# Performance work log

Measured on AMD Instinct MI355X. Metric: run time of the kernel, lower is better.

## Reference

```python
import jax, jax.numpy as jnp
import numpy as np

B, T, S, E, H, L, V = 32, 64, 64, 512, 1024, 2, 32000


def setup_inputs() -> dict:
    key = jax.random.key(0)
    ks = jax.random.split(key, 20)
    std = 0.02
    inp = {
        "x": jax.random.randint(ks[0], (B, T), 0, V),
        "h0": jax.random.normal(ks[1], (L, B, H), jnp.float32) * std,
        "c0": jax.random.normal(ks[2], (L, B, H), jnp.float32) * std,
        "x_enc": jax.random.normal(ks[3], (B, S, H), jnp.float32),
        "emb": jax.random.normal(ks[4], (V, E), jnp.float32) * std,
        # layer 0: input = concat(emb, prev_out) -> E + H
        "Wih0": jax.random.normal(ks[5], (4 * H, E + H), jnp.float32) * std,
        "Whh0": jax.random.normal(ks[6], (4 * H, H), jnp.float32) * std,
        "bih0": jnp.zeros((4 * H,), jnp.float32),
        "bhh0": jnp.zeros((4 * H,), jnp.float32),
        # layer 1: input = h of layer 0 -> H
        "Wih1": jax.random.normal(ks[7], (4 * H, H), jnp.float32) * std,
        "Whh1": jax.random.normal(ks[8], (4 * H, H), jnp.float32) * std,
        "bih1": jnp.zeros((4 * H,), jnp.float32),
        "bhh1": jnp.zeros((4 * H,), jnp.float32),
        # attention linear H->H
        "Wa": jax.random.normal(ks[9], (H, H), jnp.float32) * std,
        "ba": jnp.zeros((H,), jnp.float32),
        # output linear 2H->H
        "Wl": jax.random.normal(ks[10], (H, 2 * H), jnp.float32) * std,
        "bl": jnp.zeros((H,), jnp.float32),
        # generator H->V
        "Wg": jax.random.normal(ks[11], (V, H), jnp.float32) * std,
        "bg": jnp.zeros((V,), jnp.float32),
    }
    return inp


def _decoder_fwd(x, h0, c0, x_enc, emb, Wih0, Whh0, bih0, bhh0,
                 Wih1, Whh1, bih1, bhh1, Wa, ba, Wl, bl, Wg, bg):
    layers = ((Wih0, Whh0, bih0, bhh0), (Wih1, Whh1, bih1, bhh1))
    xs = emb[x]  # [B, T, E]

    def lstm_cell(inp, h_prev, c_prev, Wih, Whh, bih, bhh):
        g = inp @ Wih.T + bih + h_prev @ Whh.T + bhh  # [B, 4H]
        i_, f_, g_, o_ = jnp.split(g, 4, axis=-1)     # torch order: i,f,g,o
        c_new = jax.nn.sigmoid(f_) * c_prev + jax.nn.sigmoid(i_) * jnp.tanh(g_)
        h_new = jax.nn.sigmoid(o_) * jnp.tanh(c_new)
        return h_new, c_new

    def step(carry, e_t):
        h, c, prev = carry  # h,c: [L,B,H]; prev: [B,H]
        inp = jnp.concatenate([e_t, prev], axis=-1)  # [B, E+H]
        hs, cs = [], []
        for l, (Wih, Whh, bih, bhh) in enumerate(layers):
            h_new, c_new = lstm_cell(inp, h[l], c[l], Wih, Whh, bih, bhh)
            hs.append(h_new); cs.append(c_new)
            inp = h_new
        z = inp  # top-layer hidden [B, H]
        # attention: score = linear(z) . x_enc^T
        s = jnp.einsum('bh,bsh->bs', z @ Wa.T + ba, x_enc)  # [B, S]
        w = jax.nn.softmax(s, axis=-1)
        ctx = jnp.einsum('bs,bsh->bh', w, x_enc)            # [B, H]
        out = jnp.tanh(jnp.concatenate([z, ctx], axis=-1) @ Wl.T + bl)  # [B, H]
        return (jnp.stack(hs), jnp.stack(cs), out), out

    prev0 = jnp.zeros((x.shape[0], Wl.shape[0]), xs.dtype)
    e_seq = jnp.swapaxes(xs[:, :-1, :], 0, 1)  # [T-1, B, E]
    _, outs = jax.lax.scan(step, (h0, c0, prev0), e_seq)
    outs = jnp.swapaxes(outs, 0, 1)  # [B, T-1, H]
    # dropout p=0.0 (eval) -> identity; generator: linear + log_softmax
    return jax.nn.log_softmax(outs @ Wg.T + bg, axis=-1)  # [B, T-1, V]


def reference(x, h0, c0, x_enc, emb, Wih0, Whh0, bih0, bhh0,
              Wih1, Whh1, bih1, bhh1, Wa, ba, Wl, bl, Wg, bg):
    return _decoder_fwd(x, h0, c0, x_enc, emb, Wih0, Whh0, bih0, bhh0,
                        Wih1, Whh1, bih1, bhh1, Wa, ba, Wl, bl, Wg, bg)
```

## Files before the change

### kernel.cpp

```cpp
#include <hip/hip_runtime.h>
#include <hip/hip_cooperative_groups.h>
#include <math.h>

namespace cg = cooperative_groups;

#define BB 32
#define HH 1024
#define EE 512
#define TT 63
#define SS 64
#define VV 32000

static const size_t OWT0 = 0;
static const size_t OWT1 = 10485760;
static const size_t OWLT = 18874368;
static const size_t OXC0 = 20971520;
static const size_t OXC1 = 26214400;
static const size_t OGP  = 30408704;
static const size_t OOP  = 34603008;
static const size_t OPE  = 35651584;
static const size_t OCB  = 37748736;

__device__ __forceinline__ void fma4(float4& a, float s, const float4 w) {
    a.x = fmaf(s, w.x, a.x);
    a.y = fmaf(s, w.y, a.y);
    a.z = fmaf(s, w.z, a.z);
    a.w = fmaf(s, w.w, a.w);
}

template<int WPITCH, int NRT>
__device__ __forceinline__ void pgemm(const float* __restrict__ W,
                                      const float* __restrict__ X, int xpitch,
                                      int kslice, float* __restrict__ P)
{
    const int tid = threadIdx.x, lane = tid & 63, wv = tid >> 6;
    const int nU = NRT * 32;
    for (int u = blockIdx.x; u < nU; u += gridDim.x) {
        const int rt = u >> 5, kg = u & 31;
        const int r0 = rt * 256 + lane * 4;
        const int b0 = wv * 8;
        const int kbase = kg * kslice;
        const float* wb = W + (size_t)kbase * WPITCH + r0;
        const float* xb = X + (size_t)b0 * xpitch + kbase;
        float4 acc[8];
        #pragma unroll
        for (int i = 0; i < 8; ++i) acc[i] = make_float4(0.f, 0.f, 0.f, 0.f);
        #pragma unroll 2
        for (int kk = 0; kk < kslice; kk += 4) {
            float4 w0 = *(const float4*)(wb + (size_t)(kk + 0) * WPITCH);
            float4 w1 = *(const float4*)(wb + (size_t)(kk + 1) * WPITCH);
            float4 w2 = *(const float4*)(wb + (size_t)(kk + 2) * WPITCH);
            float4 w3 = *(const float4*)(wb + (size_t)(kk + 3) * WPITCH);
            #pragma unroll
            for (int i = 0; i < 8; ++i) {
                float4 xv = *(const float4*)(xb + (size_t)i * xpitch + kk);
                fma4(acc[i], xv.x, w0);
                fma4(acc[i], xv.y, w1);
                fma4(acc[i], xv.z, w2);
                fma4(acc[i], xv.w, w3);
            }
        }
        float* pp = P + ((size_t)kg * BB + b0) * WPITCH + r0;
        #pragma unroll
        for (int i = 0; i < 8; ++i) *(float4*)(pp + (size_t)i * WPITCH) = acc[i];
    }
}

__device__ __forceinline__ void lstm_fin(const float* __restrict__ P,
    const float* __restrict__ bih, const float* __restrict__ bhh,
    float* __restrict__ cst,
    float* __restrict__ hA, int pA, int oA,
    float* __restrict__ hB, int pB, int oB,
    float* __restrict__ smem)
{
    const int tid = threadIdx.x, lane = tid & 63, g = tid >> 6;
    for (int u = blockIdx.x; u < 512; u += gridDim.x) {
        const int b = u >> 4, hc = u & 15;
        const int h = hc * 64 + lane;
        float s = 0.f;
        #pragma unroll
        for (int sl = 0; sl < 32; ++sl)
            s += P[((size_t)sl * BB + b) * 4096 + g * 1024 + h];
        s += bih[g * 1024 + h] + bhh[g * 1024 + h];
        smem[g * 64 + lane] = s;
        __syncthreads();
        if (tid < 64) {
            float gi = smem[lane], gf = smem[64 + lane];
            float gg = smem[128 + lane], go = smem[192 + lane];
            float si = 1.f / (1.f + expf(-gi));
            float sf = 1.f / (1.f + expf(-gf));
            float so = 1.f / (1.f + expf(-go));
            float cp = cst[(size_t)b * 1024 + h];
            float cn = sf * cp + si * tanhf(gg);
            float hn = so * tanhf(cn);
            cst[(size_t)b * 1024 + h] = cn;
            hA[(size_t)b * pA + oA + h] = hn;
            hB[(size_t)b * pB + oB + h] = hn;
        }
        __syncthreads();
    }
}

__device__ __forceinline__ void attn_phase(const float* __restrict__ xenc,
    const float* __restrict__ pe, const float* __restrict__ cb,
    float* __restrict__ zc, float* __restrict__ smem)
{
    const int tid = threadIdx.x;
    float* zl = smem;
    float* pp = smem + 1024;
    float* wt = smem + 1280;
    for (int u = blockIdx.x; u < 32; u += gridDim.x) {
        const int b = u;
        for (int i = tid; i < 1024; i += 256) zl[i] = zc[(size_t)b * 2048 + i];
        __syncthreads();
        {
            const int j = tid >> 2, part = tid & 3;
            const float* per = pe + ((size_t)b * 64 + j) * 1024 + part * 256;
            const float* zp = zl + part * 256;
            float p0 = 0.f, p1 = 0.f, p2 = 0.f, p3 = 0.f;
            for (int k = 0; k < 256; k += 4) {
                p0 = fmaf(zp[k], per[k], p0);
                p1 = fmaf(zp[k + 1], per[k + 1], p1);
                p2 = fmaf(zp[k + 2], per[k + 2], p2);
                p3 = fmaf(zp[k + 3], per[k + 3], p3);
            }
            pp[tid] = (p0 + p1) + (p2 + p3);
        }
        __syncthreads();
        if (tid < 64) {
            float sc = pp[tid * 4] + pp[tid * 4 + 1] + pp[tid * 4 + 2] + pp[tid * 4 + 3]
                     + cb[b * 64 + tid];
            float m = sc;
            #pragma unroll
            for (int off = 32; off; off >>= 1) m = fmaxf(m, __shfl_xor(m, off));
            float e = expf(sc - m);
            float ss = e;
            #pragma unroll
            for (int off = 32; off; off >>= 1) ss += __shfl_xor(ss, off);
            wt[tid] = e / ss;
        }
        __syncthreads();
        for (int k = tid; k < 1024; k += 256) {
            float a = 0.f;
            const float* xe = xenc + (size_t)b * (SS * HH) + k;
            #pragma unroll 8
            for (int j = 0; j < SS; ++j) a = fmaf(wt[j], xe[(size_t)j * HH], a);
            zc[(size_t)b * 2048 + 1024 + k] = a;
        }
        __syncthreads();
    }
}

__device__ __forceinline__ void out_fin(const float* __restrict__ P,
    const float* __restrict__ bl, float* __restrict__ outs_t,
    float* __restrict__ xc0n, float* __restrict__ smem)
{
    const int tid = threadIdx.x, lane = tid & 63, wv = tid >> 6;
    for (int u = blockIdx.x; u < 512; u += gridDim.x) {
        const int b = u >> 4, nc = u & 15;
        const int n = nc * 64 + lane;
        float s = 0.f;
        #pragma unroll
        for (int q = 0; q < 8; ++q)
            s += P[((size_t)(wv * 8 + q) * BB + b) * 1024 + n];
        smem[wv * 64 + lane] = s;
        __syncthreads();
        if (tid < 64) {
            float tot = smem[lane] + smem[64 + lane] + smem[128 + lane]
                      + smem[192 + lane] + bl[n];
            float r = tanhf(tot);
            outs_t[(size_t)b * 1024 + n] = r;
            xc0n[(size_t)b * 2560 + 512 + n] = r;
        }
        __syncthreads();
    }
}

__global__ __launch_bounds__(256, 2)
void decoder_loop(const float* __restrict__ xenc,
                  const float* __restrict__ bih0, const float* __restrict__ bhh0,
                  const float* __restrict__ bih1, const float* __restrict__ bhh1,
                  const float* __restrict__ bl,
                  float* __restrict__ scratch,
                  float* __restrict__ c_state, float* __restrict__ zc,
                  float* __restrict__ outs)
{
    __shared__ float smem[1344];
    cg::grid_group grid = cg::this_grid();
    const float* WT0 = scratch + OWT0;
    const float* WT1 = scratch + OWT1;
    const float* WlT = scratch + OWLT;
    float* xcat0 = scratch + OXC0;
    float* xcat1 = scratch + OXC1;
    float* gatesP = scratch + OGP;
    float* outP = scratch + OOP;
    const float* pe = scratch + OPE;
    const float* cb = scratch + OCB;

    for (int t = 0; t < TT; ++t) {
        float* xc0t = xcat0 + (size_t)t * BB * 2560;
        float* xc0n = xcat0 + (size_t)(t + 1) * BB * 2560;
        float* xc1t = xcat1 + (size_t)t * BB * 2048;
        float* xc1n = xcat1 + (size_t)(t + 1) * BB * 2048;

        pgemm<4096, 16>(WT0, xc0t, 2560, 80, gatesP);
        grid.sync();
        lstm_fin(gatesP, bih0, bhh0, c_state,
                 xc1t, 2048, 0, xc0n, 2560, 1536, smem);
        grid.sync();
        pgemm<4096, 16>(WT1, xc1t, 2048, 64, gatesP);
        grid.sync();
        lstm_fin(gatesP, bih1, bhh1, c_state + 32768,
                 zc, 2048, 0, xc1n, 2048, 1024, smem);
        grid.sync();
        attn_phase(xenc, pe, cb, zc, smem);
        grid.sync();
        pgemm<1024, 4>(WlT, zc, 2048, 64, outP);
        grid.sync();
        out_fin(outP, bl, outs + (size_t)t * BB * HH, xc0n, smem);
        grid.sync();
    }
}

__global__ __launch_bounds__(256, 2)
void k_gate_gemm(const float* __restrict__ W, const float* __restrict__ X,
                 int xpitch, int kslice, float* __restrict__ P)
{ pgemm<4096, 16>(W, X, xpitch, kslice, P); }

__global__ __launch_bounds__(256, 2)
void k_out_gemm(const float* __restrict__ W, const float* __restrict__ X,
                float* __restrict__ P)
{ pgemm<1024, 4>(W, X, 2048, 64, P); }

__global__ __launch_bounds__(256)
void k_lstm_fin(const float* __restrict__ P, const float* __restrict__ bih,
                const float* __restrict__ bhh, float* __restrict__ cst,
                float* __restrict__ hA, int pA, int oA,
                float* __restrict__ hB, int pB, int oB)
{ __shared__ float smem[256]; lstm_fin(P, bih, bhh, cst, hA, pA, oA, hB, pB, oB, smem); }

__global__ __launch_bounds__(256)
void k_attn(const float* __restrict__ xenc, const float* __restrict__ pe,
            const float* __restrict__ cb, float* __restrict__ zc)
{ __shared__ float smem[1344]; attn_phase(xenc, pe, cb, zc, smem); }

__global__ __launch_bounds__(256)
void k_out_fin(const float* __restrict__ P, const float* __restrict__ bl,
               float* __restrict__ outs_t, float* __restrict__ xc0n)
{ __shared__ float smem[256]; out_fin(P, bl, outs_t, xc0n, smem); }

__global__ __launch_bounds__(256)
void init_kernel2(const float* __restrict__ h0, const float* __restrict__ c0,
                  float* __restrict__ c_state, float* __restrict__ xcat0,
                  float* __restrict__ xcat1)
{
    int i = blockIdx.x * 256 + threadIdx.x;
    c_state[i] = c0[i];
    int b = (i >> 10) & 31, h = i & 1023, l = i >> 15;
    if (l == 0) {
        xcat0[(size_t)b * 2560 + 1536 + h] = h0[i];
        xcat0[(size_t)b * 2560 + 512 + h] = 0.f;
    } else {
        xcat1[(size_t)b * 2048 + 1024 + h] = h0[i];
    }
}

__global__ __launch_bounds__(128)
void embed_kernel2(const int* __restrict__ x, const float* __restrict__ emb,
                   float* __restrict__ xcat0)
{
    int t = blockIdx.x >> 5, b = blockIdx.x & 31;
    int tok = x[b * 64 + t];
    const float4* src = (const float4*)(emb + (size_t)tok * EE);
    float4* dst = (float4*)(xcat0 + ((size_t)t * BB + b) * 2560);
    dst[threadIdx.x] = src[threadIdx.x];
}

__global__ __launch_bounds__(256)
void transpose_kernel(const float* __restrict__ src, int C,
                      float* __restrict__ dst, int dpitch)
{
    __shared__ float tile[32][33];
    const int tx = threadIdx.x & 31, ty = threadIdx.x >> 5;
    const int c0 = blockIdx.x * 32, r0 = blockIdx.y * 32;
    #pragma unroll
    for (int i = 0; i < 32; i += 8)
        tile[ty + i][tx] = src[(size_t)(r0 + ty + i) * C + (c0 + tx)];
    __syncthreads();
    #pragma unroll
    for (int i = 0; i < 32; i += 8)
        dst[(size_t)(c0 + ty + i) * dpitch + (r0 + tx)] = tile[tx][ty + i];
}

__global__ __launch_bounds__(256)
void projenc_kernel(const float* __restrict__ xenc, const float* __restrict__ Wa,
                    float* __restrict__ pe)
{
    const int r = blockIdx.x;
    const int n0 = threadIdx.x * 4;
    const float* xe = xenc + (size_t)r * HH;
    float4 a = make_float4(0.f, 0.f, 0.f, 0.f);
    for (int h = 0; h < HH; h += 4) {
        float4 xv = *(const float4*)(xe + h);
        fma4(a, xv.x, *(const float4*)(Wa + (size_t)h * HH + n0));
        fma4(a, xv.y, *(const float4*)(Wa + (size_t)(h + 1) * HH + n0));
        fma4(a, xv.z, *(const float4*)(Wa + (size_t)(h + 2) * HH + n0));
        fma4(a, xv.w, *(const float4*)(Wa + (size_t)(h + 3) * HH + n0));
    }
    *(float4*)(pe + (size_t)r * HH + n0) = a;
}

__global__ __launch_bounds__(64)
void cbias_kernel(const float* __restrict__ xenc, const float* __restrict__ ba,
                  float* __restrict__ cb)
{
    const int r = blockIdx.x;
    const float* xe = xenc + (size_t)r * HH;
    float s = 0.f;
    for (int k = threadIdx.x; k < HH; k += 64) s = fmaf(ba[k], xe[k], s);
    #pragma unroll
    for (int off = 32; off; off >>= 1) s += __shfl_xor(s, off);
    if (threadIdx.x == 0) cb[r] = s;
}

__global__ __launch_bounds__(256)
void gen_gemm_kernel(const float* __restrict__ outs, const float* __restrict__ Wg,
                     const float* __restrict__ bg, float* __restrict__ out)
{
    __shared__ float As[32 * 68];
    __shared__ float Bs[64 * 68];
    const int tid = threadIdx.x;
    const int tn = tid & 15, tm = tid >> 4;
    const int vbase = blockIdx.x * 64;
    const int rbase = blockIdx.y * 32;
    float acc[2][4] = {};

    const int arow = tid >> 3;
    const int acol = (tid & 7) * 8;
    int rg = rbase + arow;
    int ab = rg / TT, at = rg % TT;
    const float* asrc = outs + ((size_t)at * BB + ab) * HH + acol;
    const int brow = tid >> 2;
    const int bcol = (tid & 3) * 16;
    const float* bsrc = Wg + (size_t)(vbase + brow) * HH + bcol;

    for (int k0 = 0; k0 < HH; k0 += 64) {
        float4 a4a = *(const float4*)(asrc + k0);
        float4 a4b = *(const float4*)(asrc + k0 + 4);
        *(float4*)&As[arow * 68 + acol] = a4a;
        *(float4*)&As[arow * 68 + acol + 4] = a4b;
        float4 q0 = *(const float4*)(bsrc + k0);
        float4 q1 = *(const float4*)(bsrc + k0 + 4);
        float4 q2 = *(const float4*)(bsrc + k0 + 8);
        float4 q3 = *(const float4*)(bsrc + k0 + 12);
        *(float4*)&Bs[brow * 68 + bcol] = q0;
        *(float4*)&Bs[brow * 68 + bcol + 4] = q1;
        *(float4*)&Bs[brow * 68 + bcol + 8] = q2;
        *(float4*)&Bs[brow * 68 + bcol + 12] = q3;
        __syncthreads();
        #pragma unroll
        for (int k = 0; k < 64; k += 4) {
            float4 a0 = *(const float4*)&As[(tm * 2 + 0) * 68 + k];
            float4 a1 = *(const float4*)&As[(tm * 2 + 1) * 68 + k];
            float4 b0 = *(const float4*)&Bs[(tn * 4 + 0) * 68 + k];
            float4 b1 = *(const float4*)&Bs[(tn * 4 + 1) * 68 + k];
            float4 b2 = *(const float4*)&Bs[(tn * 4 + 2) * 68 + k];
            float4 b3 = *(const float4*)&Bs[(tn * 4 + 3) * 68 + k];
            acc[0][0] += a0.x * b0.x + a0.y * b0.y + a0.z * b0.z + a0.w * b0.w;
            acc[0][1] += a0.x * b1.x + a0.y * b1.y + a0.z * b1.z + a0.w * b1.w;
            acc[0][2] += a0.x * b2.x + a0.y * b2.y + a0.z * b2.z + a0.w * b2.w;
            acc[0][3] += a0.x * b3.x + a0.y * b3.y + a0.z * b3.z + a0.w * b3.w;
            acc[1][0] += a1.x * b0.x + a1.y * b0.y + a1.z * b0.z + a1.w * b0.w;
            acc[1][1] += a1.x * b1.x + a1.y * b1.y + a1.z * b1.z + a1.w * b1.w;
            acc[1][2] += a1.x * b2.x + a1.y * b2.y + a1.z * b2.z + a1.w * b2.w;
            acc[1][3] += a1.x * b3.x + a1.y * b3.y + a1.z * b3.z + a1.w * b3.w;
        }
        __syncthreads();
    }
    #pragma unroll
    for (int i = 0; i < 2; ++i) {
        int r = rbase + tm * 2 + i;
        #pragma unroll
        for (int jj = 0; jj < 4; ++jj) {
            int v = vbase + tn * 4 + jj;
            out[(size_t)r * VV + v] = acc[i][jj] + bg[v];
        }
    }
}

__global__ __launch_bounds__(256)
void logsoftmax_kernel(float* __restrict__ out)
{
    __shared__ float red[4];
    __shared__ float red2[4];
    const int tid = threadIdx.x;
    float* row = out + (size_t)blockIdx.x * VV;
    float m = -1e30f;
    for (int i = tid; i < VV; i += 256) m = fmaxf(m, row[i]);
    for (int off = 32; off; off >>= 1) m = fmaxf(m, __shfl_xor(m, off));
    if ((tid & 63) == 0) red[tid >> 6] = m;
    __syncthreads();
    m = fmaxf(fmaxf(red[0], red[1]), fmaxf(red[2], red[3]));
    float s = 0.f;
    for (int i = tid; i < VV; i += 256) s += expf(row[i] - m);
    for (int off = 32; off; off >>= 1) s += __shfl_xor(s, off);
    if ((tid & 63) == 0) red2[tid >> 6] = s;
    __syncthreads();
    s = red2[0] + red2[1] + red2[2] + red2[3];
    float lse = m + logf(s);
    for (int i = tid; i < VV; i += 256) row[i] = row[i] - lse;
}

extern "C" void kernel_launch(void* const* d_in, const int* in_sizes, int n_in,
                              void* d_out, int out_size, void* d_ws, size_t ws_size,
                              hipStream_t stream)
{
    (void)in_sizes; (void)n_in; (void)out_size; (void)ws_size;
    const int*   x    = (const int*)  d_in[0];
    const float* h0   = (const float*)d_in[1];
    const float* c0   = (const float*)d_in[2];
    const float* x_enc= (const float*)d_in[3];
    const float* emb  = (const float*)d_in[4];
    const float* Wih0 = (const float*)d_in[5];
    const float* Whh0 = (const float*)d_in[6];
    const float* bih0 = (const float*)d_in[7];
    const float* bhh0 = (const float*)d_in[8];
    const float* Wih1 = (const float*)d_in[9];
    const float* Whh1 = (const float*)d_in[10];
    const float* bih1 = (const float*)d_in[11];
    const float* bhh1 = (const float*)d_in[12];
    const float* Wa   = (const float*)d_in[13];
    const float* ba   = (const float*)d_in[14];
    const float* Wl   = (const float*)d_in[15];
    const float* bl   = (const float*)d_in[16];
    const float* Wg   = (const float*)d_in[17];
    const float* bg   = (const float*)d_in[18];
    float* out = (float*)d_out;
    float* scratch = (float*)d_out;

    float* ws      = (float*)d_ws;
    float* c_state = ws;
    float* zc      = ws + 65536;
    float* outs    = ws + 131072;

    init_kernel2<<<256, 256, 0, stream>>>(h0, c0, c_state,
                                          scratch + OXC0, scratch + OXC1);
    embed_kernel2<<<TT * BB, 128, 0, stream>>>(x, emb, scratch + OXC0);
    transpose_kernel<<<dim3(48, 128), 256, 0, stream>>>(Wih0, 1536, scratch + OWT0, 4096);
    transpose_kernel<<<dim3(32, 128), 256, 0, stream>>>(Whh0, 1024,
                         scratch + OWT0 + (size_t)1536 * 4096, 4096);
    transpose_kernel<<<dim3(32, 128), 256, 0, stream>>>(Wih1, 1024, scratch + OWT1, 4096);
    transpose_kernel<<<dim3(32, 128), 256, 0, stream>>>(Whh1, 1024,
                         scratch + OWT1 + (size_t)1024 * 4096, 4096);
    transpose_kernel<<<dim3(64, 32), 256, 0, stream>>>(Wl, 2048, scratch + OWLT, 1024);
    projenc_kernel<<<2048, 256, 0, stream>>>(x_enc, Wa, scratch + OPE);
    cbias_kernel<<<2048, 64, 0, stream>>>(x_enc, ba, scratch + OCB);

    static int coopGrid = -2;
    if (coopGrid == -2) {
        int dev = 0; hipGetDevice(&dev);
        int coop = 0;
        hipDeviceGetAttribute(&coop, hipDeviceAttributeCooperativeLaunch, dev);
        if (!coop) coopGrid = 0;
        else {
            int occ = 0;
            if (hipOccupancyMaxActiveBlocksPerMultiprocessor(&occ, decoder_loop,
                    256, 0) != hipSuccess || occ < 1) occ = 0;
            int nCU = 256;
            hipDeviceProp_t prop;
            if (hipGetDeviceProperties(&prop, dev) == hipSuccess && prop.multiProcessorCount > 0)
                nCU = prop.multiProcessorCount;
            int g = occ * nCU;
            if (g > 512) g = 512;
            coopGrid = g;
        }
    }

    bool done = false;
    if (coopGrid > 0) {
        void* args[] = {(void*)&x_enc, (void*)&bih0, (void*)&bhh0, (void*)&bih1,
                        (void*)&bhh1, (void*)&bl, (void*)&scratch, (void*)&c_state,
                        (void*)&zc, (void*)&outs};
        hipError_t e = hipLaunchCooperativeKernel(decoder_loop, dim3(coopGrid),
                                                  dim3(256), args, 0u, stream);
        if (e == hipSuccess) done = true;
        else coopGrid = 0;
    }
    if (!done) {
        for (int t = 0; t < TT; ++t) {
            float* xc0t = scratch + OXC0 + (size_t)t * BB * 2560;
            float* xc0n = scratch + OXC0 + (size_t)(t + 1) * BB * 2560;
            float* xc1t = scratch + OXC1 + (size_t)t * BB * 2048;
            float* xc1n = scratch + OXC1 + (size_t)(t + 1) * BB * 2048;
            k_gate_gemm<<<512, 256, 0, stream>>>(scratch + OWT0, xc0t, 2560, 80, scratch + OGP);
            k_lstm_fin<<<512, 256, 0, stream>>>(scratch + OGP, bih0, bhh0, c_state,
                                                xc1t, 2048, 0, xc0n, 2560, 1536);
            k_gate_gemm<<<512, 256, 0, stream>>>(scratch + OWT1, xc1t, 2048, 64, scratch + OGP);
            k_lstm_fin<<<512, 256, 0, stream>>>(scratch + OGP, bih1, bhh1, c_state + 32768,
                                                zc, 2048, 0, xc1n, 2048, 1024);
            k_attn<<<32, 256, 0, stream>>>(x_enc, scratch + OPE, scratch + OCB, zc);
            k_out_gemm<<<128, 256, 0, stream>>>(scratch + OWLT, zc, scratch + OOP);
            k_out_fin<<<512, 256, 0, stream>>>(scratch + OOP, bl,
                                               outs + (size_t)t * BB * HH, xc0n);
        }
    }

    gen_gemm_kernel<<<dim3(VV / 64, 2016 / 32), 256, 0, stream>>>(outs, Wg, bg, out);
    logsoftmax_kernel<<<2016, 256, 0, stream>>>(out);
}
```

Baseline: 24.13 ms.

## Fuse gate GEMM with LSTM cell and replace grid.sync with custom barrier

Each block now computes complete gate rows (i,f,g,o for two hidden units across all 32 batches) using untransposed weights, so the LSTM nonlinearity runs in the same phase without split-K partial buffers. This removes the partial-sum reduction phases and half of the grid-wide syncs per step, and drops the weight transpose kernels. The cooperative-groups grid.sync is replaced by a hand-rolled atomic counter barrier with relaxed agent-scope loads and stores. The risks are that each block streams full weight rows with less K-parallelism, and that relaxed atomics with no fences may not order memory correctly across blocks.

```diff
diff --git a/kernel.cpp b/kernel.cpp
--- a/kernel.cpp
+++ b/kernel.cpp
@@ -1,8 +1,5 @@
 #include <hip/hip_runtime.h>
-#include <hip/hip_cooperative_groups.h>
 #include <math.h>
-
-namespace cg = cooperative_groups;
 
 #define BB 32
 #define HH 1024
@@ -11,106 +8,163 @@
 #define SS 64
 #define VV 32000
 
-static const size_t OWT0 = 0;
-static const size_t OWT1 = 10485760;
-static const size_t OWLT = 18874368;
-static const size_t OXC0 = 20971520;
-static const size_t OXC1 = 26214400;
-static const size_t OGP  = 30408704;
-static const size_t OOP  = 34603008;
-static const size_t OPE  = 35651584;
-static const size_t OCB  = 37748736;
-
-__device__ __forceinline__ void fma4(float4& a, float s, const float4 w) {
-    a.x = fmaf(s, w.x, a.x);
-    a.y = fmaf(s, w.y, a.y);
-    a.z = fmaf(s, w.z, a.z);
-    a.w = fmaf(s, w.w, a.w);
-}
-
-template<int WPITCH, int NRT>
-__device__ __forceinline__ void pgemm(const float* __restrict__ W,
-                                      const float* __restrict__ X, int xpitch,
-                                      int kslice, float* __restrict__ P)
-{
-    const int tid = threadIdx.x, lane = tid & 63, wv = tid >> 6;
-    const int nU = NRT * 32;
-    for (int u = blockIdx.x; u < nU; u += gridDim.x) {
-        const int rt = u >> 5, kg = u & 31;
-        const int r0 = rt * 256 + lane * 4;
-        const int b0 = wv * 8;
-        const int kbase = kg * kslice;
-        const float* wb = W + (size_t)kbase * WPITCH + r0;
-        const float* xb = X + (size_t)b0 * xpitch + kbase;
-        float4 acc[8];
-        #pragma unroll
-        for (int i = 0; i < 8; ++i) acc[i] = make_float4(0.f, 0.f, 0.f, 0.f);
-        #pragma unroll 2
-        for (int kk = 0; kk < kslice; kk += 4) {
-            float4 w0 = *(const float4*)(wb + (size_t)(kk + 0) * WPITCH);
-            float4 w1 = *(const float4*)(wb + (size_t)(kk + 1) * WPITCH);
-            float4 w2 = *(const float4*)(wb + (size_t)(kk + 2) * WPITCH);
-            float4 w3 = *(const float4*)(wb + (size_t)(kk + 3) * WPITCH);
+#define OXC0 0u
+#define OXC1 5242880u
+#define OZC  9437184u
+#define OPE  13565952u
+#define OCB  15663104u
+
+#define WS_OUTS  65536u
+#define WS_FLAGS 2129920u
+
+__device__ __forceinline__ void st_dev(float* p, float v) {
+    __hip_atomic_store(p, v, __ATOMIC_RELAXED, __HIP_MEMORY_SCOPE_AGENT);
+}
+__device__ __forceinline__ float ld_dev(const float* p) {
+    return __hip_atomic_load(p, __ATOMIC_RELAXED, __HIP_MEMORY_SCOPE_AGENT);
+}
+
+__device__ __forceinline__ void gbar(unsigned* flags, int nblk, unsigned idx)
+{
+    __syncthreads();
+    if (threadIdx.x == 0) {
+        unsigned* ctr = flags;
+        unsigned* gen = flags + 32;
+        unsigned old = __hip_atomic_fetch_add(ctr, 1u, __ATOMIC_RELAXED,
+                                              __HIP_MEMORY_SCOPE_AGENT);
+        unsigned want = idx + 1u;
+        if (old == want * (unsigned)nblk - 1u) {
+            __hip_atomic_store(gen, want, __ATOMIC_RELAXED, __HIP_MEMORY_SCOPE_AGENT);
+        } else {
+            while (__hip_atomic_load(gen, __ATOMIC_RELAXED,
+                                     __HIP_MEMORY_SCOPE_AGENT) < want)
+                __builtin_amdgcn_s_sleep(8);
+        }
+    }
+    __syncthreads();
+}
+
+__device__ void lstm_phase(const float* __restrict__ Wx, int K1,
+                           const float* __restrict__ Wh,
+                           const float* __restrict__ bih, const float* __restrict__ bhh,
+                           const float* __restrict__ xc, int xpitch,
+                           float* __restrict__ cst,
+                           float* dA, int pA, int oA,
+                           float* dB, int pB, int oB,
+                           float* smem, int nblk)
+{
+    float4* lds4 = (float4*)smem;
+    float* gx = smem + 8192;
+    const int tid = threadIdx.x;
+    const int b = tid & 31, hl = (tid >> 5) & 1, gate = tid >> 6;
+    const int K = K1 + HH;
+    for (int u = blockIdx.x; u < 512; u += nblk) {
+        const int h = u * 2 + hl;
+        const int row = gate * HH + h;
+        float4 acc = make_float4(0.f, 0.f, 0.f, 0.f);
+        for (int c = 0; c < K / 256; ++c) {
+            const int k0 = c * 256;
+            __syncthreads();
             #pragma unroll
             for (int i = 0; i < 8; ++i) {
-                float4 xv = *(const float4*)(xb + (size_t)i * xpitch + kk);
-                fma4(acc[i], xv.x, w0);
-                fma4(acc[i], xv.y, w1);
-                fma4(acc[i], xv.z, w2);
-                fma4(acc[i], xv.w, w3);
+                int idx = tid + i * 256;
+                int bb = idx >> 6, kq = idx & 63;
+                float4 v = *(const float4*)(xc + (size_t)bb * xpitch + k0 + kq * 4);
+                lds4[kq * 32 + ((bb + kq) & 31)] = v;
             }
-        }
-        float* pp = P + ((size_t)kg * BB + b0) * WPITCH + r0;
-        #pragma unroll
-        for (int i = 0; i < 8; ++i) *(float4*)(pp + (size_t)i * WPITCH) = acc[i];
-    }
-}
-
-__device__ __forceinline__ void lstm_fin(const float* __restrict__ P,
-    const float* __restrict__ bih, const float* __restrict__ bhh,
-    float* __restrict__ cst,
-    float* __restrict__ hA, int pA, int oA,
-    float* __restrict__ hB, int pB, int oB,
-    float* __restrict__ smem)
-{
-    const int tid = threadIdx.x, lane = tid & 63, g = tid >> 6;
-    for (int u = blockIdx.x; u < 512; u += gridDim.x) {
-        const int b = u >> 4, hc = u & 15;
-        const int h = hc * 64 + lane;
-        float s = 0.f;
-        #pragma unroll
-        for (int sl = 0; sl < 32; ++sl)
-            s += P[((size_t)sl * BB + b) * 4096 + g * 1024 + h];
-        s += bih[g * 1024 + h] + bhh[g * 1024 + h];
-        smem[g * 64 + lane] = s;
+            __syncthreads();
+            const float* wr = (k0 < K1) ? Wx + (size_t)row * K1 + k0
+                                        : Wh + (size_t)row * HH + (k0 - K1);
+            #pragma unroll 8
+            for (int k = 0; k < 256; k += 4) {
+                const int kq = k >> 2;
+                float4 w4 = *(const float4*)(wr + k);
+                float4 xq = lds4[kq * 32 + ((b + kq) & 31)];
+                acc.x = fmaf(xq.x, w4.x, acc.x);
+                acc.y = fmaf(xq.y, w4.y, acc.y);
+                acc.z = fmaf(xq.z, w4.z, acc.z);
+                acc.w = fmaf(xq.w, w4.w, acc.w);
+            }
+        }
+        float d = (acc.x + acc.y) + (acc.z + acc.w) + bih[row] + bhh[row];
+        __syncthreads();
+        gx[gate * 64 + hl * 32 + b] = d;
         __syncthreads();
         if (tid < 64) {
-            float gi = smem[lane], gf = smem[64 + lane];
-            float gg = smem[128 + lane], go = smem[192 + lane];
+            float gi = gx[tid], gf = gx[64 + tid];
+            float gg = gx[128 + tid], go = gx[192 + tid];
             float si = 1.f / (1.f + expf(-gi));
             float sf = 1.f / (1.f + expf(-gf));
             float so = 1.f / (1.f + expf(-go));
-            float cp = cst[(size_t)b * 1024 + h];
+            float cp = ld_dev(cst + (size_t)b * HH + h);
             float cn = sf * cp + si * tanhf(gg);
             float hn = so * tanhf(cn);
-            cst[(size_t)b * 1024 + h] = cn;
-            hA[(size_t)b * pA + oA + h] = hn;
-            hB[(size_t)b * pB + oB + h] = hn;
-        }
-        __syncthreads();
-    }
-}
-
-__device__ __forceinline__ void attn_phase(const float* __restrict__ xenc,
-    const float* __restrict__ pe, const float* __restrict__ cb,
-    float* __restrict__ zc, float* __restrict__ smem)
-{
+            st_dev(cst + (size_t)b * HH + h, cn);
+            st_dev(dA + (size_t)b * pA + oA + h, hn);
+            st_dev(dB + (size_t)b * pB + oB + h, hn);
+        }
+    }
+}
+
+__device__ void outlin_phase(const float* __restrict__ Wl, const float* __restrict__ bl,
+                             const float* __restrict__ zc,
+                             float* __restrict__ outs_t, float* __restrict__ xc0n,
+                             float* smem, int nblk)
+{
+    float4* lds4 = (float4*)smem;
+    float* gx = smem + 8192;
     const int tid = threadIdx.x;
+    const int b = tid & 31, nl = (tid >> 5) & 1, q = tid >> 6;
+    for (int u = blockIdx.x; u < 512; u += nblk) {
+        const int n = u * 2 + nl;
+        float4 acc = make_float4(0.f, 0.f, 0.f, 0.f);
+        for (int c = 0; c < 8; ++c) {
+            const int k0 = c * 256;
+            __syncthreads();
+            #pragma unroll
+            for (int i = 0; i < 8; ++i) {
+                int idx = tid + i * 256;
+                int bb = idx >> 6, kq = idx & 63;
+                float4 v = *(const float4*)(zc + (size_t)bb * 2048 + k0 + kq * 4);
+                lds4[kq * 32 + ((bb + kq) & 31)] = v;
+            }
+            __syncthreads();
+            const float* wr = Wl + (size_t)n * 2048 + k0 + q * 64;
+            #pragma unroll
+            for (int k = 0; k < 64; k += 4) {
+                const int kq = (q * 64 + k) >> 2;
+                float4 w4 = *(const float4*)(wr + k);
+                float4 xq = lds4[kq * 32 + ((b + kq) & 31)];
+                acc.x = fmaf(xq.x, w4.x, acc.x);
+                acc.y = fmaf(xq.y, w4.y, acc.y);
+                acc.z = fmaf(xq.z, w4.z, acc.z);
+                acc.w = fmaf(xq.w, w4.w, acc.w);
+            }
+        }
+        float part = (acc.x + acc.y) + (acc.z + acc.w);
+        __syncthreads();
+        gx[q * 64 + nl * 32 + b] = part;
+        __syncthreads();
+        if (tid < 64) {
+            float tot = gx[tid] + gx[64 + tid] + gx[128 + tid] + gx[192 + tid] + bl[n];
+            float r = tanhf(tot);
+            st_dev(outs_t + (size_t)b * HH + n, r);
+            st_dev(xc0n + (size_t)b * 2560 + 512 + n, r);
+        }
+    }
+}
+
+__device__ void attn_phase(const float* __restrict__ xenc, const float* __restrict__ pe,
+                           const float* __restrict__ cb, float* __restrict__ zc,
+                           float* smem, int nblk)
+{
     float* zl = smem;
     float* pp = smem + 1024;
     float* wt = smem + 1280;
-    for (int u = blockIdx.x; u < 32; u += gridDim.x) {
+    const int tid = threadIdx.x;
+    for (int u = blockIdx.x; u < 32; u += nblk) {
         const int b = u;
+        __syncthreads();
         for (int i = tid; i < 1024; i += 256) zl[i] = zc[(size_t)b * 2048 + i];
         __syncthreads();
         {
@@ -145,151 +199,105 @@
             const float* xe = xenc + (size_t)b * (SS * HH) + k;
             #pragma unroll 8
             for (int j = 0; j < SS; ++j) a = fmaf(wt[j], xe[(size_t)j * HH], a);
-            zc[(size_t)b * 2048 + 1024 + k] = a;
-        }
-        __syncthreads();
-    }
-}
-
-__device__ __forceinline__ void out_fin(const float* __restrict__ P,
-    const float* __restrict__ bl, float* __restrict__ outs_t,
-    float* __restrict__ xc0n, float* __restrict__ smem)
-{
-    const int tid = threadIdx.x, lane = tid & 63, wv = tid >> 6;
-    for (int u = blockIdx.x; u < 512; u += gridDim.x) {
-        const int b = u >> 4, nc = u & 15;
-        const int n = nc * 64 + lane;
-        float s = 0.f;
-        #pragma unroll
-        for (int q = 0; q < 8; ++q)
-            s += P[((size_t)(wv * 8 + q) * BB + b) * 1024 + n];
-        smem[wv * 64 + lane] = s;
-        __syncthreads();
-        if (tid < 64) {
-            float tot = smem[lane] + smem[64 + lane] + smem[128 + lane]
-                      + smem[192 + lane] + bl[n];
-            float r = tanhf(tot);
-            outs_t[(size_t)b * 1024 + n] = r;
-            xc0n[(size_t)b * 2560 + 512 + n] = r;
+            st_dev(zc + (size_t)b * 2048 + 1024 + k, a);
         }
         __syncthreads();
     }
 }
 
 __global__ __launch_bounds__(256, 2)
-void decoder_loop(const float* __restrict__ xenc,
+void decoder_loop(const float* __restrict__ Wih0, const float* __restrict__ Whh0,
                   const float* __restrict__ bih0, const float* __restrict__ bhh0,
+                  const float* __restrict__ Wih1, const float* __restrict__ Whh1,
                   const float* __restrict__ bih1, const float* __restrict__ bhh1,
-                  const float* __restrict__ bl,
-                  float* __restrict__ scratch,
-                  float* __restrict__ c_state, float* __restrict__ zc,
-                  float* __restrict__ outs)
-{
-    __shared__ float smem[1344];
-    cg::grid_group grid = cg::this_grid();
-    const float* WT0 = scratch + OWT0;
-    const float* WT1 = scratch + OWT1;
-    const float* WlT = scratch + OWLT;
-    float* xcat0 = scratch + OXC0;
-    float* xcat1 = scratch + OXC1;
-    float* gatesP = scratch + OGP;
-    float* outP = scratch + OOP;
+                  const float* __restrict__ Wl, const float* __restrict__ bl,
+                  const float* __restrict__ xenc,
+                  float* __restrict__ scratch, float* __restrict__ cst,
+                  float* __restrict__ outs, unsigned* __restrict__ flags)
+{
+    __shared__ __align__(16) float smem[8448];
+    const int nblk = gridDim.x;
+    float* xc0 = scratch + OXC0;
+    float* xc1 = scratch + OXC1;
+    float* zct = scratch + OZC;
     const float* pe = scratch + OPE;
     const float* cb = scratch + OCB;
-
+    unsigned bi = 0;
     for (int t = 0; t < TT; ++t) {
-        float* xc0t = xcat0 + (size_t)t * BB * 2560;
-        float* xc0n = xcat0 + (size_t)(t + 1) * BB * 2560;
-        float* xc1t = xcat1 + (size_t)t * BB * 2048;
-        float* xc1n = xcat1 + (size_t)(t + 1) * BB * 2048;
-
-        pgemm<4096, 16>(WT0, xc0t, 2560, 80, gatesP);
-        grid.sync();
-        lstm_fin(gatesP, bih0, bhh0, c_state,
-                 xc1t, 2048, 0, xc0n, 2560, 1536, smem);
-        grid.sync();
-        pgemm<4096, 16>(WT1, xc1t, 2048, 64, gatesP);
-        grid.sync();
-        lstm_fin(gatesP, bih1, bhh1, c_state + 32768,
-                 zc, 2048, 0, xc1n, 2048, 1024, smem);
-        grid.sync();
-        attn_phase(xenc, pe, cb, zc, smem);
-        grid.sync();
-        pgemm<1024, 4>(WlT, zc, 2048, 64, outP);
-        grid.sync();
-        out_fin(outP, bl, outs + (size_t)t * BB * HH, xc0n, smem);
-        grid.sync();
+        float* xc0t = xc0 + (size_t)t * BB * 2560;
+        float* xc0n = xc0 + (size_t)(t + 1) * BB * 2560;
+        float* xc1t = xc1 + (size_t)t * BB * 2048;
+        float* xc1n = xc1 + (size_t)(t + 1) * BB * 2048;
+        float* zc   = zct + (size_t)t * BB * 2048;
+
+        lstm_phase(Wih0, 1536, Whh0, bih0, bhh0, xc0t, 2560, cst,
+                   xc1t, 2048, 0, xc0n, 2560, 1536, smem, nblk);
+        gbar(flags, nblk, bi++);
+        lstm_phase(Wih1, 1024, Whh1, bih1, bhh1, xc1t, 2048, cst + 32768,
+                   zc, 2048, 0, xc1n, 2048, 1024, smem, nblk);
+        gbar(flags, nblk, bi++);
+        attn_phase(xenc, pe, cb, zc, smem, nblk);
+        gbar(flags, nblk, bi++);
+        outlin_phase(Wl, bl, zc, outs + (size_t)t * BB * HH, xc0n, smem, nblk);
+        gbar(flags, nblk, bi++);
     }
 }
 
 __global__ __launch_bounds__(256, 2)
-void k_gate_gemm(const float* __restrict__ W, const float* __restrict__ X,
-                 int xpitch, int kslice, float* __restrict__ P)
-{ pgemm<4096, 16>(W, X, xpitch, kslice, P); }
-
+void k_lstm(const float* Wx, int K1, const float* Wh,
+            const float* bih, const float* bhh,
+            const float* xc, int xpitch, float* cst,
+            float* dA, int pA, int oA, float* dB, int pB, int oB)
+{
+    __shared__ __align__(16) float smem[8448];
+    lstm_phase(Wx, K1, Wh, bih, bhh, xc, xpitch, cst, dA, pA, oA, dB, pB, oB,
+               smem, gridDim.x);
+}
 __global__ __launch_bounds__(256, 2)
-void k_out_gemm(const float* __restrict__ W, const float* __restrict__ X,
-                float* __restrict__ P)
-{ pgemm<1024, 4>(W, X, 2048, 64, P); }
-
-__global__ __launch_bounds__(256)
-void k_lstm_fin(const float* __restrict__ P, const float* __restrict__ bih,
-                const float* __restrict__ bhh, float* __restrict__ cst,
-                float* __restrict__ hA, int pA, int oA,
-                float* __restrict__ hB, int pB, int oB)
-{ __shared__ float smem[256]; lstm_fin(P, bih, bhh, cst, hA, pA, oA, hB, pB, oB, smem); }
-
-__global__ __launch_bounds__(256)
-void k_attn(const float* __restrict__ xenc, const float* __restrict__ pe,
-            const float* __restrict__ cb, float* __restrict__ zc)
-{ __shared__ float smem[1344]; attn_phase(xenc, pe, cb, zc, smem); }
-
-__global__ __launch_bounds__(256)
-void k_out_fin(const float* __restrict__ P, const float* __restrict__ bl,
-               float* __restrict__ outs_t, float* __restrict__ xc0n)
-{ __shared__ float smem[256]; out_fin(P, bl, outs_t, xc0n, smem); }
+void k_attn(const float* xenc, const float* pe, const float* cb, float* zc)
+{
+    __shared__ __align__(16) float smem[8448];
+    attn_phase(xenc, pe, cb, zc, smem, gridDim.x);
+}
+__global__ __launch_bounds__(256, 2)
+void k_outlin(const float* Wl, const float* bl, const float* zc,
+              float* outs_t, float* xc0n)
+{
+    __shared__ __align__(16) float smem[8448];
+    outlin_phase(Wl, bl, zc, outs_t, xc0n, smem, gridDim.x);
+}
 
 __global__ __launch_bounds__(256)
 void init_kernel2(const float* __restrict__ h0, const float* __restrict__ c0,
-                  float* __restrict__ c_state, float* __restrict__ xcat0,
-                  float* __restrict__ xcat1)
+                  float* __restrict__ cst, float* __restrict__ xc0,
+                  float* __restrict__ xc1, unsigned* __restrict__ flags)
 {
     int i = blockIdx.x * 256 + threadIdx.x;
-    c_state[i] = c0[i];
-    int b = (i >> 10) & 31, h = i & 1023, l = i >> 15;
+    cst[i] = c0[i];
+    int l = i >> 15, b = (i >> 10) & 31, h = i & 1023;
     if (l == 0) {
-        xcat0[(size_t)b * 2560 + 1536 + h] = h0[i];
-        xcat0[(size_t)b * 2560 + 512 + h] = 0.f;
+        xc0[(size_t)b * 2560 + 1536 + h] = h0[i];
+        xc0[(size_t)b * 2560 + 512 + h] = 0.f;
     } else {
-        xcat1[(size_t)b * 2048 + 1024 + h] = h0[i];
-    }
+        xc1[(size_t)b * 2048 + 1024 + h] = h0[i];
+    }
+    if (i < 64) flags[i] = 0u;
 }
 
 __global__ __launch_bounds__(128)
 void embed_kernel2(const int* __restrict__ x, const float* __restrict__ emb,
-                   float* __restrict__ xcat0)
+                   float* __restrict__ xc0)
 {
     int t = blockIdx.x >> 5, b = blockIdx.x & 31;
     int tok = x[b * 64 + t];
     const float4* src = (const float4*)(emb + (size_t)tok * EE);
-    float4* dst = (float4*)(xcat0 + ((size_t)t * BB + b) * 2560);
+    float4* dst = (float4*)(xc0 + ((size_t)t * BB + b) * 2560);
     dst[threadIdx.x] = src[threadIdx.x];
 }
 
-__global__ __launch_bounds__(256)
-void transpose_kernel(const float* __restrict__ src, int C,
-                      float* __restrict__ dst, int dpitch)
-{
-    __shared__ float tile[32][33];
-    const int tx = threadIdx.x & 31, ty = threadIdx.x >> 5;
-    const int c0 = blockIdx.x * 32, r0 = blockIdx.y * 32;
-    #pragma unroll
-    for (int i = 0; i < 32; i += 8)
-        tile[ty + i][tx] = src[(size_t)(r0 + ty + i) * C + (c0 + tx)];
-    __syncthreads();
-    #pragma unroll
-    for (int i = 0; i < 32; i += 8)
-        dst[(size_t)(c0 + ty + i) * dpitch + (r0 + tx)] = tile[tx][ty + i];
+__device__ __forceinline__ void fma4h(float4& a, float s, const float4 w) {
+    a.x = fmaf(s, w.x, a.x); a.y = fmaf(s, w.y, a.y);
+    a.z = fmaf(s, w.z, a.z); a.w = fmaf(s, w.w, a.w);
 }
 
 __global__ __launch_bounds__(256)
@@ -302,10 +310,10 @@
     float4 a = make_float4(0.f, 0.f, 0.f, 0.f);
     for (int h = 0; h < HH; h += 4) {
         float4 xv = *(const float4*)(xe + h);
-        fma4(a, xv.x, *(const float4*)(Wa + (size_t)h * HH + n0));
-        fma4(a, xv.y, *(const float4*)(Wa + (size_t)(h + 1) * HH + n0));
-        fma4(a, xv.z, *(const float4*)(Wa + (size_t)(h + 2) * HH + n0));
-        fma4(a, xv.w, *(const float4*)(Wa + (size_t)(h + 3) * HH + n0));
+        fma4h(a, xv.x, *(const float4*)(Wa + (size_t)h * HH + n0));
+        fma4h(a, xv.y, *(const float4*)(Wa + (size_t)(h + 1) * HH + n0));
+        fma4h(a, xv.z, *(const float4*)(Wa + (size_t)(h + 2) * HH + n0));
+        fma4h(a, xv.w, *(const float4*)(Wa + (size_t)(h + 3) * HH + n0));
     }
     *(float4*)(pe + (size_t)r * HH + n0) = a;
 }
@@ -438,23 +446,21 @@
     float* out = (float*)d_out;
     float* scratch = (float*)d_out;
 
-    float* ws      = (float*)d_ws;
-    float* c_state = ws;
-    float* zc      = ws + 65536;
-    float* outs    = ws + 131072;
-
-    init_kernel2<<<256, 256, 0, stream>>>(h0, c0, c_state,
-                                          scratch + OXC0, scratch + OXC1);
-    embed_kernel2<<<TT * BB, 128, 0, stream>>>(x, emb, scratch + OXC0);
-    transpose_kernel<<<dim3(48, 128), 256, 0, stream>>>(Wih0, 1536, scratch + OWT0, 4096);
-    transpose_kernel<<<dim3(32, 128), 256, 0, stream>>>(Whh0, 1024,
-                         scratch + OWT0 + (size_t)1536 * 4096, 4096);
-    transpose_kernel<<<dim3(32, 128), 256, 0, stream>>>(Wih1, 1024, scratch + OWT1, 4096);
-    transpose_kernel<<<dim3(32, 128), 256, 0, stream>>>(Whh1, 1024,
-                         scratch + OWT1 + (size_t)1024 * 4096, 4096);
-    transpose_kernel<<<dim3(64, 32), 256, 0, stream>>>(Wl, 2048, scratch + OWLT, 1024);
-    projenc_kernel<<<2048, 256, 0, stream>>>(x_enc, Wa, scratch + OPE);
-    cbias_kernel<<<2048, 64, 0, stream>>>(x_enc, ba, scratch + OCB);
+    float* ws    = (float*)d_ws;
+    float* cst   = ws;
+    float* outs  = ws + WS_OUTS;
+    unsigned* flags = (unsigned*)(ws + WS_FLAGS);
+
+    float* xc0 = scratch + OXC0;
+    float* xc1 = scratch + OXC1;
+    float* zct = scratch + OZC;
+    float* pe  = scratch + OPE;
+    float* cb  = scratch + OCB;
+
+    init_kernel2<<<256, 256, 0, stream>>>(h0, c0, cst, xc0, xc1, flags);
+    embed_kernel2<<<TT * BB, 128, 0, stream>>>(x, emb, xc0);
+    projenc_kernel<<<2048, 256, 0, stream>>>(x_enc, Wa, pe);
+    cbias_kernel<<<2048, 64, 0, stream>>>(x_enc, ba, cb);
 
     static int coopGrid = -2;
     if (coopGrid == -2) {
@@ -468,7 +474,8 @@
                     256, 0) != hipSuccess || occ < 1) occ = 0;
             int nCU = 256;
             hipDeviceProp_t prop;
-            if (hipGetDeviceProperties(&prop, dev) == hipSuccess && prop.multiProcessorCount > 0)
+            if (hipGetDeviceProperties(&prop, dev) == hipSuccess &&
+                prop.multiProcessorCount > 0)
                 nCU = prop.multiProcessorCount;
             int g = occ * nCU;
             if (g > 512) g = 512;
@@ -478,9 +485,10 @@
 
     bool done = false;
     if (coopGrid > 0) {
-        void* args[] = {(void*)&x_enc, (void*)&bih0, (void*)&bhh0, (void*)&bih1,
-                        (void*)&bhh1, (void*)&bl, (void*)&scratch, (void*)&c_state,
-                        (void*)&zc, (void*)&outs};
+        void* args[] = {(void*)&Wih0, (void*)&Whh0, (void*)&bih0, (void*)&bhh0,
+                        (void*)&Wih1, (void*)&Whh1, (void*)&bih1, (void*)&bhh1,
+                        (void*)&Wl, (void*)&bl, (void*)&x_enc,
+                        (void*)&scratch, (void*)&cst, (void*)&outs, (void*)&flags};
         hipError_t e = hipLaunchCooperativeKernel(decoder_loop, dim3(coopGrid),
                                                   dim3(256), args, 0u, stream);
         if (e == hipSuccess) done = true;
@@ -488,20 +496,18 @@
     }
     if (!done) {
         for (int t = 0; t < TT; ++t) {
-            float* xc0t = scratch + OXC0 + (size_t)t * BB * 2560;
-            float* xc0n = scratch + OXC0 + (size_t)(t + 1) * BB * 2560;
-            float* xc1t = scratch + OXC1 + (size_t)t * BB * 2048;
-            float* xc1n = scratch + OXC1 + (size_t)(t + 1) * BB * 2048;
-            k_gate_gemm<<<512, 256, 0, stream>>>(scratch + OWT0, xc0t, 2560, 80, scratch + OGP);
-            k_lstm_fin<<<512, 256, 0, stream>>>(scratch + OGP, bih0, bhh0, c_state,
-                                                xc1t, 2048, 0, xc0n, 2560, 1536);
-            k_gate_gemm<<<512, 256, 0, stream>>>(scratch + OWT1, xc1t, 2048, 64, scratch + OGP);
-            k_lstm_fin<<<512, 256, 0, stream>>>(scratch + OGP, bih1, bhh1, c_state + 32768,
-                                                zc, 2048, 0, xc1n, 2048, 1024);
-            k_attn<<<32, 256, 0, stream>>>(x_enc, scratch + OPE, scratch + OCB, zc);
-            k_out_gemm<<<128, 256, 0, stream>>>(scratch + OWLT, zc, scratch + OOP);
-            k_out_fin<<<512, 256, 0, stream>>>(scratch + OOP, bl,
-                                               outs + (size_t)t * BB * HH, xc0n);
+            float* xc0t = xc0 + (size_t)t * BB * 2560;
+            float* xc0n = xc0 + (size_t)(t + 1) * BB * 2560;
+            float* xc1t = xc1 + (size_t)t * BB * 2048;
+            float* xc1n = xc1 + (size_t)(t + 1) * BB * 2048;
+            float* zc   = zct + (size_t)t * BB * 2048;
+            k_lstm<<<512, 256, 0, stream>>>(Wih0, 1536, Whh0, bih0, bhh0,
+                xc0t, 2560, cst, xc1t, 2048, 0, xc0n, 2560, 1536);
+            k_lstm<<<512, 256, 0, stream>>>(Wih1, 1024, Whh1, bih1, bhh1,
+                xc1t, 2048, cst + 32768, zc, 2048, 0, xc1n, 2048, 1024);
+            k_attn<<<32, 256, 0, stream>>>(x_enc, pe, cb, zc);
+            k_outlin<<<512, 256, 0, stream>>>(Wl, bl, zc,
+                outs + (size_t)t * BB * HH, xc0n);
         }
     }
 
```

New measurement: 22.60 ms. -6.4%, faster.
